# Kernel optimization log

Measured on AMD Instinct MI355X. Metric: run time of the kernel, lower is better.

Reference implementation:

```python
import jax, jax.numpy as jnp
import numpy as np
import math

H = 16          # num heads
D = 64          # head dim
MAX_POS = 512   # max_position_embeddings


def setup_inputs() -> dict:
    key = jax.random.key(0)
    ks = jax.random.split(key, 8)
    B, S, E = 8, 512, 1024
    scale = 1.0 / math.sqrt(E)
    return {
        "hidden_states": jax.random.normal(ks[0], (B, S, E), jnp.float32),
        "attention_mask": jnp.zeros((B, 1, 1, S), jnp.float32),
        "Wq": jax.random.normal(ks[1], (E, E), jnp.float32) * scale,
        "bq": jnp.zeros((E,), jnp.float32),
        "Wk": jax.random.normal(ks[2], (E, E), jnp.float32) * scale,
        "bk": jnp.zeros((E,), jnp.float32),
        "Wv": jax.random.normal(ks[3], (E, E), jnp.float32) * scale,
        "bv": jnp.zeros((E,), jnp.float32),
        "dist_emb": jax.random.normal(ks[4], (2 * MAX_POS - 1, D), jnp.float32) * 0.02,
    }


def reference(hidden_states, attention_mask, Wq, bq, Wk, bk, Wv, bv, dist_emb):
    B, S, E = hidden_states.shape

    def heads(x):  # [B,S,E] -> [B,H,S,D]
        return x.reshape(B, S, H, D).transpose(0, 2, 1, 3)

    q = heads(hidden_states @ Wq + bq)
    k = heads(hidden_states @ Wk + bk)
    v = heads(hidden_states @ Wv + bv)

    # raw scores [B,H,S,S]
    scores = jnp.einsum('bhld,bhrd->bhlr', q, k)

    # relative position embedding lookup: distance[l,r] = l - r
    pos = jnp.arange(S)
    distance = pos[:, None] - pos[None, :]               # [S,S]
    pe = dist_emb[distance + MAX_POS - 1]                # [S,S,D]
    scores = scores + jnp.einsum('bhld,lrd->bhlr', q, pe)
    scores = scores + jnp.einsum('bhrd,lrd->bhlr', k, pe)

    scores = scores / math.sqrt(D) + attention_mask
    probs = jax.nn.softmax(scores, axis=-1)

    ctx = jnp.einsum('bhlr,bhrd->bhld', probs, v)        # [B,H,S,D]
    ctx = ctx.transpose(0, 2, 1, 3).reshape(B, S, H * D)
    return ctx
```

## Files before the change

kernel.cpp:

```cpp
#include <hip/hip_runtime.h>

#define BATCH 8
#define SEQ   512
#define EMB   1024
#define NH    16
#define HD    64

typedef __bf16 bf16x8 __attribute__((ext_vector_type(8)));
typedef float  f32x4  __attribute__((ext_vector_type(4)));

__device__ __forceinline__ unsigned short f2bf(float f){
  return __builtin_bit_cast(unsigned short, (__bf16)f);
}
__device__ __forceinline__ float bf2f(unsigned short s){
  union { unsigned u; float f; } v; v.u = ((unsigned)s) << 16;
  return v.f;
}

__device__ __forceinline__ float dpp_max16(float x){
  int t;
  t = __builtin_amdgcn_update_dpp(0, __builtin_bit_cast(int, x), 0xB1, 0xF, 0xF, true);
  x = fmaxf(x, __builtin_bit_cast(float, t));
  t = __builtin_amdgcn_update_dpp(0, __builtin_bit_cast(int, x), 0x4E, 0xF, 0xF, true);
  x = fmaxf(x, __builtin_bit_cast(float, t));
  t = __builtin_amdgcn_update_dpp(0, __builtin_bit_cast(int, x), 0x141, 0xF, 0xF, true);
  x = fmaxf(x, __builtin_bit_cast(float, t));
  t = __builtin_amdgcn_update_dpp(0, __builtin_bit_cast(int, x), 0x140, 0xF, 0xF, true);
  x = fmaxf(x, __builtin_bit_cast(float, t));
  return x;
}
__device__ __forceinline__ float dpp_sum16(float x){
  int t;
  t = __builtin_amdgcn_update_dpp(0, __builtin_bit_cast(int, x), 0xB1, 0xF, 0xF, true);
  x += __builtin_bit_cast(float, t);
  t = __builtin_amdgcn_update_dpp(0, __builtin_bit_cast(int, x), 0x4E, 0xF, 0xF, true);
  x += __builtin_bit_cast(float, t);
  t = __builtin_amdgcn_update_dpp(0, __builtin_bit_cast(int, x), 0x141, 0xF, 0xF, true);
  x += __builtin_bit_cast(float, t);
  t = __builtin_amdgcn_update_dpp(0, __builtin_bit_cast(int, x), 0x140, 0xF, 0xF, true);
  x += __builtin_bit_cast(float, t);
  return x;
}

__device__ __forceinline__ int swzc(int row, int chunk){
  return row * 128 + (((chunk ^ (row & 7)) & 7) << 4);
}
__device__ __forceinline__ int swz2(int row, int col){
  return row * 128 + ((((col >> 3) ^ (row & 7)) & 7) << 4) + ((col & 7) << 1);
}

__device__ __forceinline__ void gload16(const unsigned short* g, unsigned char* lds){
  __builtin_amdgcn_global_load_lds((const __attribute__((address_space(1))) unsigned int*)g,
                                   (__attribute__((address_space(3))) unsigned int*)lds,
                                   16, 0, 0);
}

__device__ __forceinline__ void bar_lds(){
  asm volatile("s_waitcnt lgkmcnt(0)" ::: "memory");
  __builtin_amdgcn_s_barrier();
}

__global__ void k_pre(const float* __restrict__ hid, unsigned short* __restrict__ hidb,
                      const float* __restrict__ dist, unsigned short* __restrict__ distb,
                      const float* __restrict__ Wq, const float* __restrict__ Wk,
                      const float* __restrict__ Wv, unsigned short* __restrict__ wqt,
                      unsigned short* __restrict__ wkt, unsigned short* __restrict__ wvt){
  int bid = blockIdx.x;
  int t = threadIdx.x;
  if (bid < 4096){
    int i = (bid * 256 + t) * 4;
    float4 v = *(const float4*)(hid + i);
    ushort4 o; o.x = f2bf(v.x); o.y = f2bf(v.y); o.z = f2bf(v.z); o.w = f2bf(v.w);
    *(ushort4*)(hidb + i) = o;
  } else if (bid < 4352){
    int i = (bid - 4096) * 256 + t;
    distb[i] = (i < 1023 * 64) ? f2bf(dist[i]) : (unsigned short)0;
  } else {
    int wt = bid - 4352;
    int z = wt >> 10, rem = wt & 1023;
    const float* W = (z == 0) ? Wq : (z == 1) ? Wk : Wv;
    unsigned short* WT = (z == 0) ? wqt : (z == 1) ? wkt : wvt;
    __shared__ float tl[32][33];
    int n0 = (rem & 31) * 32, k0 = (rem >> 5) * 32;
    int tx = t & 31, ty = t >> 5;
#pragma unroll
    for (int i = 0; i < 4; i++)
      tl[ty + 8*i][tx] = W[(k0 + ty + 8*i) * EMB + n0 + tx];
    __syncthreads();
#pragma unroll
    for (int i = 0; i < 4; i++)
      WT[(n0 + ty + 8*i) * EMB + k0 + tx] = f2bf(tl[tx][ty + 8*i]);
  }
}

__global__ __launch_bounds__(256, 3) void k_gemm3(const unsigned short* __restrict__ A,
                                                  const unsigned short* __restrict__ wqt,
                                                  const unsigned short* __restrict__ wkt,
                                                  const unsigned short* __restrict__ wvt,
                                                  const float* __restrict__ bq,
                                                  const float* __restrict__ bk,
                                                  const float* __restrict__ bv,
                                                  unsigned short* __restrict__ qb,
                                                  unsigned short* __restrict__ kb,
                                                  unsigned short* __restrict__ vtb){
  int z = blockIdx.z;
  const unsigned short* BT = (z == 0) ? wqt : (z == 1) ? wkt : wvt;
  const float* bias = (z == 0) ? bq : (z == 1) ? bk : bv;
  unsigned short* out = (z == 0) ? qb : (z == 1) ? kb : vtb;
  int mode = (z == 2);

  __shared__ __align__(16) unsigned char sA[128 * 128];
  __shared__ __align__(16) unsigned char sB[128 * 128];
  int m0 = blockIdx.y * 128, n0 = blockIdx.x * 128;
  int t = threadIdx.x, w = t >> 6, lane = t & 63, g = lane >> 4, lr = lane & 15;
  int rowbase = (w >> 1) * 64, colbase = (w & 1) * 64;
  int lrow = lane >> 3, lc = lane & 7;
  f32x4 acc[4][4] = {};
  for (int k0 = 0; k0 < EMB; k0 += 64){
    __syncthreads();
#pragma unroll
    for (int i = 0; i < 4; i++){
      int row = (w + 4*i) * 8 + lrow;
      int cg  = lc ^ (row & 7);
      gload16(A  + (m0 + row) * EMB + k0 + cg*8, sA + (w + 4*i) * 1024);
      gload16(BT + (n0 + row) * EMB + k0 + cg*8, sB + (w + 4*i) * 1024);
    }
    __syncthreads();
#pragma unroll
    for (int kk = 0; kk < 2; kk++){
      bf16x8 af[4], bfv[4];
#pragma unroll
      for (int i = 0; i < 4; i++) af[i]  = *(const bf16x8*)(sA + swzc(rowbase + 16*i + lr, kk*4 + g));
#pragma unroll
      for (int j = 0; j < 4; j++) bfv[j] = *(const bf16x8*)(sB + swzc(colbase + 16*j + lr, kk*4 + g));
#pragma unroll
      for (int i = 0; i < 4; i++)
#pragma unroll
        for (int j = 0; j < 4; j++)
          acc[i][j] = __builtin_amdgcn_mfma_f32_16x16x32_bf16(af[i], bfv[j], acc[i][j], 0, 0, 0);
    }
  }
#pragma unroll
  for (int i = 0; i < 4; i++)
#pragma unroll
    for (int j = 0; j < 4; j++)
#pragma unroll
      for (int r = 0; r < 4; r++){
        int m = m0 + rowbase + 16*i + 4*g + r;
        int n = n0 + colbase + 16*j + lr;
        float val = acc[i][j][r] + bias[n];
        int b = m >> 9, s = m & 511, h = n >> 6, d = n & 63;
        int idx = (mode == 0) ? (((b*NH + h)*SEQ + s)*HD + d)
                              : (((b*NH + h)*HD + d)*SEQ + s);
        out[idx] = f2bf(val);
      }
}

__global__ __launch_bounds__(512, 2) void k_attn(const unsigned short* __restrict__ qb,
                                                 const unsigned short* __restrict__ kb,
                                                 const unsigned short* __restrict__ vtb,
                                                 const unsigned short* __restrict__ distb,
                                                 const float* __restrict__ mask,
                                                 float* __restrict__ out){
  __shared__ __align__(16) unsigned char sK[2][64 * 128];
  __shared__ __align__(16) unsigned char sV[2][64 * 128];
  __shared__ __align__(16) unsigned char sSA[8][2624];
  __shared__ __align__(16) unsigned char sSB[8][2560];

  const float SCL  = 0.125f * 1.4426950408889634f;
  const float L2E  = 1.4426950408889634f;

  int bid = blockIdx.x;
  int wgid = (bid & 7) * 64 + (bid >> 3);
  int lt = wgid & 3, h = (wgid >> 2) & 15, b = wgid >> 6;
  int L0 = lt * 128;
  int bh = b * NH + h;
  int t = threadIdx.x, w = t >> 6, lane = t & 63, g = lane >> 4, lr = lane & 15;
  int lbase = 16 * w;
  unsigned char* mySA = sSA[w];
  unsigned char* mySB = sSB[w];
  unsigned char* myP  = mySA;
  const float* maskp = mask + b * SEQ;

  const unsigned short* qrow = qb + (bh * SEQ + L0 + lbase + lr) * HD + 8 * g;
  bf16x8 aq0 = *(const bf16x8*)qrow;
  bf16x8 aq1 = *(const bf16x8*)(qrow + 32);

  bf16x8 pe[5][2];
#define LOAD_PE(JB) do {                                                     \
    const unsigned short* _pb = distb + ((JB) + 16*w + lr) * HD + 8*g;       \
    _Pragma("unroll")                                                        \
    for (int _j = 0; _j < 5; _j++){                                          \
      pe[_j][0] = *(const bf16x8*)(_pb + _j*16*HD);                          \
      pe[_j][1] = *(const bf16x8*)(_pb + _j*16*HD + 32); }                   \
  } while(0)

  int lrow = lane >> 3, lc = lane & 7;
  int row0 = w * 8 + lrow;
  int cg0  = lc ^ (row0 & 7);
  const unsigned short* kbase = kb  + bh * SEQ * HD;
  const unsigned short* vbase = vtb + bh * HD * SEQ;

  uint4 kst0 = *(const uint4*)(kbase + row0 * HD  + cg0 * 8);
  uint4 vst0 = *(const uint4*)(vbase + row0 * SEQ + cg0 * 8);
  *(uint4*)(sK[0] + w * 1024 + lane * 16) = kst0;
  *(uint4*)(sV[0] + w * 1024 + lane * 16) = vst0;
  kst0 = *(const uint4*)(kbase + 64 * HD + row0 * HD  + cg0 * 8);
  vst0 = *(const uint4*)(vbase + 64      + row0 * SEQ + cg0 * 8);
  LOAD_PE(L0 + 448);

  f32x4 o[4] = {};
  float mrun[4], srun[4];
#pragma unroll
  for (int r = 0; r < 4; r++){ mrun[r] = -1e30f; srun[r] = 0.f; }

  for (int rt = 0; rt < 8; rt++){
    int R0 = rt * 64;
    int cur = rt & 1, nxt = cur ^ 1;

    bar_lds();

    if (rt < 7){
      *(uint4*)(sK[nxt] + w * 1024 + lane * 16) = kst0;
      *(uint4*)(sV[nxt] + w * 1024 + lane * 16) = vst0;
    }
    if (rt < 6){
      kst0 = *(const uint4*)(kbase + (R0 + 128) * HD + row0 * HD  + cg0 * 8);
      vst0 = *(const uint4*)(vbase + (R0 + 128)      + row0 * SEQ + cg0 * 8);
    }

    float mreg[4];
#pragma unroll
    for (int f = 0; f < 4; f++) mreg[f] = maskp[R0 + 16*f + lr];

    __builtin_amdgcn_s_setprio(1);
    f32x4 sc[4];
#pragma unroll
    for (int f = 0; f < 4; f++){
      bf16x8 k0 = *(const bf16x8*)(sK[cur] + swzc(16*f + lr, g));
      bf16x8 k1 = *(const bf16x8*)(sK[cur] + swzc(16*f + lr, 4 + g));
      f32x4 a = {};
      a = __builtin_amdgcn_mfma_f32_16x16x32_bf16(aq0, k0, a, 0, 0, 0);
      a = __builtin_amdgcn_mfma_f32_16x16x32_bf16(aq1, k1, a, 0, 0, 0);
      sc[f] = a;
      f32x4 b0 = {}, b1 = {};
      b0 = __builtin_amdgcn_mfma_f32_16x16x32_bf16(k0, pe[3 - f][0], b0, 0, 0, 0);
      b0 = __builtin_amdgcn_mfma_f32_16x16x32_bf16(k1, pe[3 - f][1], b0, 0, 0, 0);
      b1 = __builtin_amdgcn_mfma_f32_16x16x32_bf16(k0, pe[4 - f][0], b1, 0, 0, 0);
      b1 = __builtin_amdgcn_mfma_f32_16x16x32_bf16(k1, pe[4 - f][1], b1, 0, 0, 0);
#pragma unroll
      for (int reg = 0; reg < 4; reg++){
        int ss = 4*g + reg + lr;
        float v = (ss >= 15) ? b0[reg] : b1[reg];
        int row = 16*f + 4*g + reg;
        int col = (ss + 1) & 15;
        *(__bf16*)(mySB + row*40 + col*2) = (__bf16)v;
      }
    }

#pragma unroll
    for (int jt2 = 0; jt2 < 5; jt2++){
      f32x4 a = {};
      a = __builtin_amdgcn_mfma_f32_16x16x32_bf16(aq0, pe[jt2][0], a, 0, 0, 0);
      a = __builtin_amdgcn_mfma_f32_16x16x32_bf16(aq1, pe[jt2][1], a, 0, 0, 0);
#pragma unroll
      for (int reg = 0; reg < 4; reg++){
        int rloc = 63 + 4*g + reg - lr - 16*jt2;
        int addr = ((unsigned)rloc < 64u) ? (rloc*40 + (4*g + reg)*2) : 2560;
        *(__bf16*)(mySA + addr) = (__bf16)a[reg];
      }
    }
    __builtin_amdgcn_s_setprio(0);

    if (rt < 7) LOAD_PE(L0 + 448 - 64*(rt + 1));

#pragma unroll
    for (int f = 0; f < 4; f++){
      ushort4 sa = *(const ushort4*)(mySA + (16*f + lr)*40 + 8*g);
      ushort4 sb = *(const ushort4*)(mySB + (16*f + lr)*40 + 8*g);
      float madd = mreg[f] * L2E;
      sc[f][0] = (sc[f][0] + bf2f(sa.x) + bf2f(sb.x)) * SCL + madd;
      sc[f][1] = (sc[f][1] + bf2f(sa.y) + bf2f(sb.y)) * SCL + madd;
      sc[f][2] = (sc[f][2] + bf2f(sa.z) + bf2f(sb.z)) * SCL + madd;
      sc[f][3] = (sc[f][3] + bf2f(sa.w) + bf2f(sb.w)) * SCL + madd;
    }

    float fac[4];
#pragma unroll
    for (int r = 0; r < 4; r++){
      float tm = fmaxf(fmaxf(sc[0][r], sc[1][r]), fmaxf(sc[2][r], sc[3][r]));
      tm = dpp_max16(tm);
      float mnew = fmaxf(mrun[r], tm);
      float fr = exp2f(mrun[r] - mnew);
      float ps = 0.f;
#pragma unroll
      for (int f = 0; f < 4; f++){ float p = exp2f(sc[f][r] - mnew); sc[f][r] = p; ps += p; }
      ps = dpp_sum16(ps);
      srun[r] = srun[r] * fr + ps;
      mrun[r] = mnew;
      fac[r]  = fr;
    }
#pragma unroll
    for (int df = 0; df < 4; df++)
#pragma unroll
      for (int r = 0; r < 4; r++) o[df][r] *= fac[r];

#pragma unroll
    for (int f = 0; f < 4; f++)
#pragma unroll
      for (int r = 0; r < 4; r++)
        *(__bf16*)(myP + swz2(4*g + r, 16*f + lr)) = (__bf16)sc[f][r];

    __builtin_amdgcn_s_setprio(1);
#pragma unroll
    for (int kk = 0; kk < 2; kk++){
      bf16x8 pf = *(const bf16x8*)(myP + swzc(lr, kk*4 + g));
#pragma unroll
      for (int df = 0; df < 4; df++){
        bf16x8 vf = *(const bf16x8*)(sV[cur] + swzc(16*df + lr, kk*4 + g));
        o[df] = __builtin_amdgcn_mfma_f32_16x16x32_bf16(pf, vf, o[df], 0, 0, 0);
      }
    }
    __builtin_amdgcn_s_setprio(0);
  }

#pragma unroll
  for (int r = 0; r < 4; r++){
    float inv = 1.0f / srun[r];
#pragma unroll
    for (int df = 0; df < 4; df++){
      int l = L0 + lbase + 4*g + r;
      out[(b * SEQ + l) * EMB + h * HD + 16*df + lr] = o[df][r] * inv;
    }
  }
#undef LOAD_PE
}

extern "C" void kernel_launch(void* const* d_in, const int* in_sizes, int n_in,
                              void* d_out, int out_size, void* d_ws, size_t ws_size,
                              hipStream_t stream) {
  (void)in_sizes; (void)n_in; (void)out_size; (void)ws_size;
  const float* hid  = (const float*)d_in[0];
  const float* mask = (const float*)d_in[1];
  const float* Wq   = (const float*)d_in[2];
  const float* bq   = (const float*)d_in[3];
  const float* Wk   = (const float*)d_in[4];
  const float* bk   = (const float*)d_in[5];
  const float* Wv   = (const float*)d_in[6];
  const float* bv   = (const float*)d_in[7];
  const float* dist = (const float*)d_in[8];
  float* out = (float*)d_out;

  unsigned char* ws = (unsigned char*)d_ws;
  unsigned short* hidb  = (unsigned short*)ws;
  unsigned short* wqt   = hidb + 4096 * 1024;
  unsigned short* wkt   = wqt  + 1024 * 1024;
  unsigned short* wvt   = wkt  + 1024 * 1024;
  unsigned short* distb = wvt  + 1024 * 1024;
  unsigned short* qb    = distb + 1024 * 64;
  unsigned short* kb    = qb + BATCH * NH * SEQ * HD;
  unsigned short* vtb   = kb + BATCH * NH * SEQ * HD;

  k_pre<<<7424, 256, 0, stream>>>(hid, hidb, dist, distb, Wq, Wk, Wv, wqt, wkt, wvt);
  k_gemm3<<<dim3(8, 32, 3), 256, 0, stream>>>(hidb, wqt, wkt, wvt, bq, bk, bv, qb, kb, vtb);
  k_attn<<<512, 512, 0, stream>>>(qb, kb, vtb, distb, mask, out);
}
```

Before: 105.0 us.

## Software-pipeline attention: overlap next tile's QK/bias MFMAs with current PV

Restructures the attention kernel into a software pipeline: the score and relative-position band MFMAs for the next key tile are issued alongside the PV MFMAs of the current tile, with a prologue and epilogue added. Workgroups shrink from 8 to 4 waves covering 64 query rows, doubling the grid to 1024 blocks, and each thread now loads two K/V rows per tile. The P staging buffer moves into the current sK slot to save LDS. The aim is to hide softmax and LDS latency behind matrix work and raise occupancy, at the cost of higher register pressure, more total K/V loads across blocks, and an extra barrier per tile.

```diff
diff --git a/kernel.cpp b/kernel.cpp
--- a/kernel.cpp
+++ b/kernel.cpp
@@ -156,7 +156,7 @@
       }
 }
 
-__global__ __launch_bounds__(512, 2) void k_attn(const unsigned short* __restrict__ qb,
+__global__ __launch_bounds__(256, 2) void k_attn(const unsigned short* __restrict__ qb,
                                                  const unsigned short* __restrict__ kb,
                                                  const unsigned short* __restrict__ vtb,
                                                  const unsigned short* __restrict__ distb,
@@ -164,22 +164,21 @@
                                                  float* __restrict__ out){
   __shared__ __align__(16) unsigned char sK[2][64 * 128];
   __shared__ __align__(16) unsigned char sV[2][64 * 128];
-  __shared__ __align__(16) unsigned char sSA[8][2624];
-  __shared__ __align__(16) unsigned char sSB[8][2560];
+  __shared__ __align__(16) unsigned char sSA[4][2624];
+  __shared__ __align__(16) unsigned char sSB[4][2560];
 
   const float SCL  = 0.125f * 1.4426950408889634f;
   const float L2E  = 1.4426950408889634f;
 
   int bid = blockIdx.x;
-  int wgid = (bid & 7) * 64 + (bid >> 3);
-  int lt = wgid & 3, h = (wgid >> 2) & 15, b = wgid >> 6;
-  int L0 = lt * 128;
+  int wgid = (bid & 7) * 128 + (bid >> 3);
+  int lt = wgid & 7, h = (wgid >> 3) & 15, b = wgid >> 7;
+  int L0 = lt * 64;
   int bh = b * NH + h;
   int t = threadIdx.x, w = t >> 6, lane = t & 63, g = lane >> 4, lr = lane & 15;
   int lbase = 16 * w;
   unsigned char* mySA = sSA[w];
   unsigned char* mySB = sSB[w];
-  unsigned char* myP  = mySA;
   const float* maskp = mask + b * SEQ;
 
   const unsigned short* qrow = qb + (bh * SEQ + L0 + lbase + lr) * HD + 8 * g;
@@ -195,95 +194,96 @@
       pe[_j][1] = *(const bf16x8*)(_pb + _j*16*HD + 32); }                   \
   } while(0)
 
+#define BANDS_QK(dst, sKb) do {                                              \
+    _Pragma("unroll")                                                        \
+    for (int f = 0; f < 4; f++){                                             \
+      bf16x8 kf0 = *(const bf16x8*)((sKb) + swzc(16*f + lr, g));             \
+      bf16x8 kf1 = *(const bf16x8*)((sKb) + swzc(16*f + lr, 4 + g));         \
+      f32x4 a = {};                                                          \
+      a = __builtin_amdgcn_mfma_f32_16x16x32_bf16(aq0, kf0, a, 0, 0, 0);     \
+      a = __builtin_amdgcn_mfma_f32_16x16x32_bf16(aq1, kf1, a, 0, 0, 0);     \
+      dst[f] = a;                                                            \
+      f32x4 b0 = {}, b1 = {};                                                \
+      b0 = __builtin_amdgcn_mfma_f32_16x16x32_bf16(kf0, pe[3 - f][0], b0, 0, 0, 0); \
+      b0 = __builtin_amdgcn_mfma_f32_16x16x32_bf16(kf1, pe[3 - f][1], b0, 0, 0, 0); \
+      b1 = __builtin_amdgcn_mfma_f32_16x16x32_bf16(kf0, pe[4 - f][0], b1, 0, 0, 0); \
+      b1 = __builtin_amdgcn_mfma_f32_16x16x32_bf16(kf1, pe[4 - f][1], b1, 0, 0, 0); \
+      _Pragma("unroll")                                                      \
+      for (int reg = 0; reg < 4; reg++){                                     \
+        int ss = 4*g + reg + lr;                                             \
+        float v = (ss >= 15) ? b0[reg] : b1[reg];                            \
+        *(__bf16*)(mySB + (16*f + 4*g + reg)*40 + (((ss + 1) & 15) << 1)) = (__bf16)v; } } \
+    _Pragma("unroll")                                                        \
+    for (int jt2 = 0; jt2 < 5; jt2++){                                       \
+      f32x4 a = {};                                                          \
+      a = __builtin_amdgcn_mfma_f32_16x16x32_bf16(aq0, pe[jt2][0], a, 0, 0, 0); \
+      a = __builtin_amdgcn_mfma_f32_16x16x32_bf16(aq1, pe[jt2][1], a, 0, 0, 0); \
+      _Pragma("unroll")                                                      \
+      for (int reg = 0; reg < 4; reg++){                                     \
+        int rloc = 63 + 4*g + reg - lr - 16*jt2;                             \
+        int addr = ((unsigned)rloc < 64u) ? (rloc*40 + (4*g + reg)*2) : 2560; \
+        *(__bf16*)(mySA + addr) = (__bf16)a[reg]; } }                        \
+  } while(0)
+
+#define COMBINE(dst) do {                                                    \
+    _Pragma("unroll")                                                        \
+    for (int f = 0; f < 4; f++){                                             \
+      ushort4 sa = *(const ushort4*)(mySA + (16*f + lr)*40 + 8*g);           \
+      ushort4 sb = *(const ushort4*)(mySB + (16*f + lr)*40 + 8*g);           \
+      float madd = mreg[f] * L2E;                                            \
+      dst[f][0] = (dst[f][0] + bf2f(sa.x) + bf2f(sb.x)) * SCL + madd;        \
+      dst[f][1] = (dst[f][1] + bf2f(sa.y) + bf2f(sb.y)) * SCL + madd;        \
+      dst[f][2] = (dst[f][2] + bf2f(sa.z) + bf2f(sb.z)) * SCL + madd;        \
+      dst[f][3] = (dst[f][3] + bf2f(sa.w) + bf2f(sb.w)) * SCL + madd; }      \
+  } while(0)
+
   int lrow = lane >> 3, lc = lane & 7;
-  int row0 = w * 8 + lrow;
-  int cg0  = lc ^ (row0 & 7);
+  int row0 = w * 8 + lrow,      row1 = (w + 4) * 8 + lrow;
+  int cg0  = lc ^ (row0 & 7),   cg1  = lc ^ (row1 & 7);
   const unsigned short* kbase = kb  + bh * SEQ * HD;
   const unsigned short* vbase = vtb + bh * HD * SEQ;
 
-  uint4 kst0 = *(const uint4*)(kbase + row0 * HD  + cg0 * 8);
-  uint4 vst0 = *(const uint4*)(vbase + row0 * SEQ + cg0 * 8);
-  *(uint4*)(sK[0] + w * 1024 + lane * 16) = kst0;
-  *(uint4*)(sV[0] + w * 1024 + lane * 16) = vst0;
-  kst0 = *(const uint4*)(kbase + 64 * HD + row0 * HD  + cg0 * 8);
-  vst0 = *(const uint4*)(vbase + 64      + row0 * SEQ + cg0 * 8);
+  f32x4 o[4] = {};
+  float mrun[4], srun[4], mreg[4];
+#pragma unroll
+  for (int r = 0; r < 4; r++){ mrun[r] = -1e30f; srun[r] = 0.f; }
+
+  {
+    uint4 a0 = *(const uint4*)(kbase + row0 * HD  + cg0 * 8);
+    uint4 a1 = *(const uint4*)(kbase + row1 * HD  + cg1 * 8);
+    uint4 c0 = *(const uint4*)(vbase + row0 * SEQ + cg0 * 8);
+    uint4 c1 = *(const uint4*)(vbase + row1 * SEQ + cg1 * 8);
+    *(uint4*)(sK[0] + w * 1024 + lane * 16)       = a0;
+    *(uint4*)(sK[0] + (w + 4) * 1024 + lane * 16) = a1;
+    *(uint4*)(sV[0] + w * 1024 + lane * 16)       = c0;
+    *(uint4*)(sV[0] + (w + 4) * 1024 + lane * 16) = c1;
+  }
+  uint4 kst0 = *(const uint4*)(kbase + 64 * HD + row0 * HD  + cg0 * 8);
+  uint4 kst1 = *(const uint4*)(kbase + 64 * HD + row1 * HD  + cg1 * 8);
+  uint4 vst0 = *(const uint4*)(vbase + 64      + row0 * SEQ + cg0 * 8);
+  uint4 vst1 = *(const uint4*)(vbase + 64      + row1 * SEQ + cg1 * 8);
   LOAD_PE(L0 + 448);
-
-  f32x4 o[4] = {};
-  float mrun[4], srun[4];
-#pragma unroll
-  for (int r = 0; r < 4; r++){ mrun[r] = -1e30f; srun[r] = 0.f; }
-
-  for (int rt = 0; rt < 8; rt++){
-    int R0 = rt * 64;
+  bar_lds();
+  *(uint4*)(sK[1] + w * 1024 + lane * 16)       = kst0;
+  *(uint4*)(sK[1] + (w + 4) * 1024 + lane * 16) = kst1;
+  *(uint4*)(sV[1] + w * 1024 + lane * 16)       = vst0;
+  *(uint4*)(sV[1] + (w + 4) * 1024 + lane * 16) = vst1;
+  kst0 = *(const uint4*)(kbase + 128 * HD + row0 * HD  + cg0 * 8);
+  kst1 = *(const uint4*)(kbase + 128 * HD + row1 * HD  + cg1 * 8);
+  vst0 = *(const uint4*)(vbase + 128      + row0 * SEQ + cg0 * 8);
+  vst1 = *(const uint4*)(vbase + 128      + row1 * SEQ + cg1 * 8);
+  f32x4 sc[4];
+#pragma unroll
+  for (int f = 0; f < 4; f++) mreg[f] = maskp[16*f + lr];
+  __builtin_amdgcn_s_setprio(1);
+  BANDS_QK(sc, sK[0]);
+  __builtin_amdgcn_s_setprio(0);
+  LOAD_PE(L0 + 448 - 64);
+  COMBINE(sc);
+
+  for (int rt = 0; rt < 7; rt++){
     int cur = rt & 1, nxt = cur ^ 1;
-
     bar_lds();
-
-    if (rt < 7){
-      *(uint4*)(sK[nxt] + w * 1024 + lane * 16) = kst0;
-      *(uint4*)(sV[nxt] + w * 1024 + lane * 16) = vst0;
-    }
-    if (rt < 6){
-      kst0 = *(const uint4*)(kbase + (R0 + 128) * HD + row0 * HD  + cg0 * 8);
-      vst0 = *(const uint4*)(vbase + (R0 + 128)      + row0 * SEQ + cg0 * 8);
-    }
-
-    float mreg[4];
-#pragma unroll
-    for (int f = 0; f < 4; f++) mreg[f] = maskp[R0 + 16*f + lr];
-
-    __builtin_amdgcn_s_setprio(1);
-    f32x4 sc[4];
-#pragma unroll
-    for (int f = 0; f < 4; f++){
-      bf16x8 k0 = *(const bf16x8*)(sK[cur] + swzc(16*f + lr, g));
-      bf16x8 k1 = *(const bf16x8*)(sK[cur] + swzc(16*f + lr, 4 + g));
-      f32x4 a = {};
-      a = __builtin_amdgcn_mfma_f32_16x16x32_bf16(aq0, k0, a, 0, 0, 0);
-      a = __builtin_amdgcn_mfma_f32_16x16x32_bf16(aq1, k1, a, 0, 0, 0);
-      sc[f] = a;
-      f32x4 b0 = {}, b1 = {};
-      b0 = __builtin_amdgcn_mfma_f32_16x16x32_bf16(k0, pe[3 - f][0], b0, 0, 0, 0);
-      b0 = __builtin_amdgcn_mfma_f32_16x16x32_bf16(k1, pe[3 - f][1], b0, 0, 0, 0);
-      b1 = __builtin_amdgcn_mfma_f32_16x16x32_bf16(k0, pe[4 - f][0], b1, 0, 0, 0);
-      b1 = __builtin_amdgcn_mfma_f32_16x16x32_bf16(k1, pe[4 - f][1], b1, 0, 0, 0);
-#pragma unroll
-      for (int reg = 0; reg < 4; reg++){
-        int ss = 4*g + reg + lr;
-        float v = (ss >= 15) ? b0[reg] : b1[reg];
-        int row = 16*f + 4*g + reg;
-        int col = (ss + 1) & 15;
-        *(__bf16*)(mySB + row*40 + col*2) = (__bf16)v;
-      }
-    }
-
-#pragma unroll
-    for (int jt2 = 0; jt2 < 5; jt2++){
-      f32x4 a = {};
-      a = __builtin_amdgcn_mfma_f32_16x16x32_bf16(aq0, pe[jt2][0], a, 0, 0, 0);
-      a = __builtin_amdgcn_mfma_f32_16x16x32_bf16(aq1, pe[jt2][1], a, 0, 0, 0);
-#pragma unroll
-      for (int reg = 0; reg < 4; reg++){
-        int rloc = 63 + 4*g + reg - lr - 16*jt2;
-        int addr = ((unsigned)rloc < 64u) ? (rloc*40 + (4*g + reg)*2) : 2560;
-        *(__bf16*)(mySA + addr) = (__bf16)a[reg];
-      }
-    }
-    __builtin_amdgcn_s_setprio(0);
-
-    if (rt < 7) LOAD_PE(L0 + 448 - 64*(rt + 1));
-
-#pragma unroll
-    for (int f = 0; f < 4; f++){
-      ushort4 sa = *(const ushort4*)(mySA + (16*f + lr)*40 + 8*g);
-      ushort4 sb = *(const ushort4*)(mySB + (16*f + lr)*40 + 8*g);
-      float madd = mreg[f] * L2E;
-      sc[f][0] = (sc[f][0] + bf2f(sa.x) + bf2f(sb.x)) * SCL + madd;
-      sc[f][1] = (sc[f][1] + bf2f(sa.y) + bf2f(sb.y)) * SCL + madd;
-      sc[f][2] = (sc[f][2] + bf2f(sa.z) + bf2f(sb.z)) * SCL + madd;
-      sc[f][3] = (sc[f][3] + bf2f(sa.w) + bf2f(sb.w)) * SCL + madd;
-    }
 
     float fac[4];
 #pragma unroll
@@ -305,16 +305,24 @@
 #pragma unroll
       for (int r = 0; r < 4; r++) o[df][r] *= fac[r];
 
+    unsigned char* Pst = sK[cur] + w * 2048;
 #pragma unroll
     for (int f = 0; f < 4; f++)
 #pragma unroll
       for (int r = 0; r < 4; r++)
-        *(__bf16*)(myP + swz2(4*g + r, 16*f + lr)) = (__bf16)sc[f][r];
-
+        *(__bf16*)(Pst + swz2(4*g + r, 16*f + lr)) = (__bf16)sc[f][r];
+
+    int R0n = (rt + 1) * 64;
+#pragma unroll
+    for (int f = 0; f < 4; f++) mreg[f] = maskp[R0n + 16*f + lr];
+
+    f32x4 scn[4];
     __builtin_amdgcn_s_setprio(1);
+    BANDS_QK(scn, sK[nxt]);
+
 #pragma unroll
     for (int kk = 0; kk < 2; kk++){
-      bf16x8 pf = *(const bf16x8*)(myP + swzc(lr, kk*4 + g));
+      bf16x8 pf = *(const bf16x8*)(Pst + swzc(lr, kk*4 + g));
 #pragma unroll
       for (int df = 0; df < 4; df++){
         bf16x8 vf = *(const bf16x8*)(sV[cur] + swzc(16*df + lr, kk*4 + g));
@@ -322,6 +330,66 @@
       }
     }
     __builtin_amdgcn_s_setprio(0);
+
+    if (rt < 6) LOAD_PE(L0 + 448 - 64*(rt + 2));
+
+    COMBINE(scn);
+#pragma unroll
+    for (int f = 0; f < 4; f++) sc[f] = scn[f];
+
+    if (rt < 6){
+      bar_lds();
+      *(uint4*)(sK[cur] + w * 1024 + lane * 16)       = kst0;
+      *(uint4*)(sK[cur] + (w + 4) * 1024 + lane * 16) = kst1;
+      *(uint4*)(sV[cur] + w * 1024 + lane * 16)       = vst0;
+      *(uint4*)(sV[cur] + (w + 4) * 1024 + lane * 16) = vst1;
+      if (rt < 5){
+        int R3 = (rt + 3) * 64;
+        kst0 = *(const uint4*)(kbase + R3 * HD + row0 * HD  + cg0 * 8);
+        kst1 = *(const uint4*)(kbase + R3 * HD + row1 * HD  + cg1 * 8);
+        vst0 = *(const uint4*)(vbase + R3      + row0 * SEQ + cg0 * 8);
+        vst1 = *(const uint4*)(vbase + R3      + row1 * SEQ + cg1 * 8);
+      }
+    }
+  }
+
+  bar_lds();
+  {
+    float fac[4];
+#pragma unroll
+    for (int r = 0; r < 4; r++){
+      float tm = fmaxf(fmaxf(sc[0][r], sc[1][r]), fmaxf(sc[2][r], sc[3][r]));
+      tm = dpp_max16(tm);
+      float mnew = fmaxf(mrun[r], tm);
+      float fr = exp2f(mrun[r] - mnew);
+      float ps = 0.f;
+#pragma unroll
+      for (int f = 0; f < 4; f++){ float p = exp2f(sc[f][r] - mnew); sc[f][r] = p; ps += p; }
+      ps = dpp_sum16(ps);
+      srun[r] = srun[r] * fr + ps;
+      mrun[r] = mnew;
+      fac[r]  = fr;
+    }
+#pragma unroll
+    for (int df = 0; df < 4; df++)
+#pragma unroll
+      for (int r = 0; r < 4; r++) o[df][r] *= fac[r];
+
+    unsigned char* Pst = sK[1] + w * 2048;
+#pragma unroll
+    for (int f = 0; f < 4; f++)
+#pragma unroll
+      for (int r = 0; r < 4; r++)
+        *(__bf16*)(Pst + swz2(4*g + r, 16*f + lr)) = (__bf16)sc[f][r];
+#pragma unroll
+    for (int kk = 0; kk < 2; kk++){
+      bf16x8 pf = *(const bf16x8*)(Pst + swzc(lr, kk*4 + g));
+#pragma unroll
+      for (int df = 0; df < 4; df++){
+        bf16x8 vf = *(const bf16x8*)(sV[1] + swzc(16*df + lr, kk*4 + g));
+        o[df] = __builtin_amdgcn_mfma_f32_16x16x32_bf16(pf, vf, o[df], 0, 0, 0);
+      }
+    }
   }
 
 #pragma unroll
@@ -334,6 +402,8 @@
     }
   }
 #undef LOAD_PE
+#undef BANDS_QK
+#undef COMBINE
 }
 
 extern "C" void kernel_launch(void* const* d_in, const int* in_sizes, int n_in,
@@ -363,5 +433,5 @@
 
   k_pre<<<7424, 256, 0, stream>>>(hid, hidb, dist, distb, Wq, Wk, Wv, wqt, wkt, wvt);
   k_gemm3<<<dim3(8, 32, 3), 256, 0, stream>>>(hidb, wqt, wkt, wvt, bq, bk, bv, qb, kb, vtb);
-  k_attn<<<512, 512, 0, stream>>>(qb, kb, vtb, distb, mask, out);
-}
+  k_attn<<<1024, 256, 0, stream>>>(qb, kb, vtb, distb, mask, out);
+}
```

Result: no change. 106.5 us (+1.4%).
